# Kernel optimization log

Measured on AMD Instinct MI355X. Metric: run time of the kernel, lower is better.

The kernel has to match this reference:

```python
import jax, jax.numpy as jnp
import numpy as np

SEQ_LEN = 4096
D_IN = 2048
D_OUT = 2048
DROPOUT_P = 0.5


def setup_inputs() -> dict:
    key = jax.random.key(0)
    kx, kq, kk, kv = jax.random.split(key, 4)
    return {
        "x": jax.random.normal(kx, (SEQ_LEN, D_IN), dtype=jnp.float32),
        "W_query": jax.random.uniform(kq, (D_IN, D_OUT), dtype=jnp.float32),
        "W_key": jax.random.uniform(kk, (D_IN, D_OUT), dtype=jnp.float32),
        "W_value": jax.random.uniform(kv, (D_IN, D_OUT), dtype=jnp.float32),
    }


def reference(x, W_query, W_key, W_value):
    # projections: [S, d_in] @ [d_in, d_out] -> [S, d_out]
    queries = x @ W_query
    keys = x @ W_key
    values = x @ W_value
    # full score matrix [S, S]
    attn_scores = queries @ keys.T
    S = attn_scores.shape[0]
    causal_mask = jnp.triu(jnp.ones((S, S), dtype=bool), k=1)
    masked = jnp.where(causal_mask, -jnp.inf, attn_scores)
    scale = jnp.sqrt(jnp.asarray(keys.shape[-1], dtype=masked.dtype))
    attn_weights = jax.nn.softmax(masked / scale, axis=1)
    # dropout p=0.5 (train mode), inverted scaling, deterministic key
    keep = jax.random.bernoulli(jax.random.key(42), 1.0 - DROPOUT_P, attn_weights.shape)
    attn_weights = jnp.where(keep, attn_weights / (1.0 - DROPOUT_P), 0.0)
    context_vec = attn_weights @ values  # [S, d_out]
    return context_vec
```

## Files before the change

### kernel.cpp

```cpp
#include <hip/hip_runtime.h>
#include <cstdint>
#include <cstddef>
#include <cmath>

#define SEQ 4096
#define DM  2048
#define NSC ((SEQ / 128) * (SEQ / 128 + 1) / 2)

typedef unsigned int u32;
typedef unsigned short u16;
typedef __attribute__((ext_vector_type(8))) short bf16x8;
typedef __attribute__((ext_vector_type(4))) float f32x4;
typedef __attribute__((ext_vector_type(16))) float f32x16;

__device__ __forceinline__ u16 f2bf(float f) {
  u32 u = __float_as_uint(f);
  return (u16)((u + 0x7FFFu + ((u >> 16) & 1u)) >> 16);
}
__device__ __forceinline__ float bf2f(u16 h) { return __uint_as_float(((u32)h) << 16); }

__device__ __forceinline__ u32 rotl32(u32 x, int r) { return (x << r) | (x >> (32 - r)); }

__device__ __forceinline__ void tf2x32(u32 c0, u32 c1, u32& o0, u32& o1) {
  const u32 k0 = 0u, k1 = 42u, k2 = 0x1BD11BDAu ^ 0u ^ 42u;
  u32 x0 = c0 + k0;
  u32 x1 = c1 + k1;
#define TFR(r) { x0 += x1; x1 = rotl32(x1, (r)); x1 ^= x0; }
  TFR(13) TFR(15) TFR(26) TFR(6)   x0 += k1; x1 += k2 + 1u;
  TFR(17) TFR(29) TFR(16) TFR(24)  x0 += k2; x1 += k0 + 2u;
  TFR(13) TFR(15) TFR(26) TFR(6)   x0 += k0; x1 += k1 + 3u;
  TFR(17) TFR(29) TFR(16) TFR(24)  x0 += k1; x1 += k2 + 4u;
  TFR(13) TFR(15) TFR(26) TFR(6)   x0 += k2; x1 += k0 + 5u;
#undef TFR
  o0 = x0; o1 = x1;
}

__device__ __forceinline__ bool dropout_keep(u32 idx) {
  u32 a, b; tf2x32(0u, idx, a, b);
  return (((a ^ b) & 0x80000000u) == 0u);
}

__device__ __forceinline__ void g2l16(const void* g, void* l) {
  __builtin_amdgcn_global_load_lds((const __attribute__((address_space(1))) u32*)g,
                                   (__attribute__((address_space(3))) u32*)l, 16, 0, 0);
}

#define MFMA16(a, b, c) __builtin_amdgcn_mfma_f32_16x16x32_bf16(a, b, c, 0, 0, 0)
#define MFMA32(a, b, c) __builtin_amdgcn_mfma_f32_32x32x16_bf16(a, b, c, 0, 0, 0)


__device__ __forceinline__ void gemm_core_split(
    const u16* __restrict__ Ah, const u16* __restrict__ AlFT,
    const u16* __restrict__ Bh, const u16* __restrict__ BlFT,
    int lda, int ldb, int rowBlock, int colBlock, int kmax,
    f32x16 (&acc)[2][2], u16* smem)
{
  u16* Als = smem;
  u16* Bls = smem + 8192;
  const int tid  = threadIdx.x;
  const int wid  = tid >> 6;
  const int lane = tid & 63;
  const int wr   = (wid & 1) << 6;
  const int wc   = (wid >> 1) << 6;
  const int l31  = lane & 31;
  const int lh   = lane >> 5;
  const int srow = wid * 32 + (lane >> 2);
  const int skol = (((lane & 3) ^ ((lane >> 3) & 3)) << 3);
  const int KA16 = lda >> 4, KB16 = ldb >> 4;
  const int rtA0 = (rowBlock >> 5) + ((wid & 1) << 1);
  const int rtB0 = (colBlock >> 5) + ((wid >> 1) << 1);
  const int swz  = (l31 >> 1) & 3;

  const f32x16 zero = {0.f,0.f,0.f,0.f,0.f,0.f,0.f,0.f,0.f,0.f,0.f,0.f,0.f,0.f,0.f,0.f};
#pragma unroll
  for (int i = 0; i < 2; ++i)
#pragma unroll
    for (int j = 0; j < 2; ++j) acc[i][j] = zero;

  for (int kb = 0; kb < kmax; kb += 64) {
#pragma unroll
    for (int h = 0; h < 2; ++h)
#pragma unroll
      for (int t = 0; t < 2; ++t) {
        const size_t ga = (size_t)(rowBlock + srow + t * 16) * lda + kb + h * 32 + skol;
        const size_t gb = (size_t)(colBlock + srow + t * 16) * ldb + kb + h * 32 + skol;
        const int lo = h * 4096 + (wid * 32 + t * 16) * 32;
        g2l16(Ah + ga, &Als[lo]);
        g2l16(Bh + gb, &Bls[lo]);
      }
    __syncthreads();

#pragma unroll
    for (int q = 0; q < 4; ++q) {
      const int h = q >> 1, s = q & 1;
      const int kt16 = (kb >> 4) + q;
      const int cl = s * 2 + lh;
      bf16x8 ah[2], bh[2], al[2], bl[2];
#pragma unroll
      for (int r = 0; r < 2; ++r) {
        const int rowA = wr + r * 32 + l31;
        const int rowB = wc + r * 32 + l31;
        ah[r] = *(const bf16x8*)&Als[h * 4096 + rowA * 32 + ((cl ^ swz) << 3)];
        bh[r] = *(const bf16x8*)&Bls[h * 4096 + rowB * 32 + ((cl ^ swz) << 3)];
        al[r] = *(const bf16x8*)(AlFT + (((size_t)(rtA0 + r) * KA16 + kt16) * 64 + lane) * 8);
        bl[r] = *(const bf16x8*)(BlFT + (((size_t)(rtB0 + r) * KB16 + kt16) * 64 + lane) * 8);
      }
#pragma unroll
      for (int r = 0; r < 2; ++r)
#pragma unroll
        for (int c = 0; c < 2; ++c) {
          acc[r][c] = MFMA32(ah[r], bh[c], acc[r][c]);
          acc[r][c] = MFMA32(ah[r], bl[c], acc[r][c]);
          acc[r][c] = MFMA32(al[r], bh[c], acc[r][c]);
        }
    }
    __syncthreads();
  }
}

__device__ __forceinline__ void gemm_core(
    const u16* __restrict__ Ah, const u16* __restrict__ Bh,
    int lda, int ldb, int rowBlock, int colBlock, int kmax,
    f32x4 (&acc)[4][4], u16* smem)
{
  u16* Als = smem;
  u16* Bls = smem + 8192;
  const int tid  = threadIdx.x;
  const int wid  = tid >> 6;
  const int lane = tid & 63;
  const int wr   = (wid & 1) << 6;
  const int wc   = (wid >> 1) << 6;
  const int lrow = lane & 15;
  const int lk   = (((lane >> 4) ^ ((lrow >> 1) & 3)) << 3);
  const int srow = wid * 32 + (lane >> 2);
  const int skol = (((lane & 3) ^ ((lane >> 3) & 3)) << 3);

  const f32x4 zero = {0.f, 0.f, 0.f, 0.f};
#pragma unroll
  for (int i = 0; i < 4; ++i)
#pragma unroll
    for (int j = 0; j < 4; ++j) acc[i][j] = zero;

  for (int kb = 0; kb < kmax; kb += 64) {
#pragma unroll
    for (int h = 0; h < 2; ++h)
#pragma unroll
      for (int t = 0; t < 2; ++t) {
        const size_t ga = (size_t)(rowBlock + srow + t * 16) * lda + kb + h * 32 + skol;
        const size_t gb = (size_t)(colBlock + srow + t * 16) * ldb + kb + h * 32 + skol;
        const int lo = h * 4096 + (wid * 32 + t * 16) * 32;
        g2l16(Ah + ga, &Als[lo]);
        g2l16(Bh + gb, &Bls[lo]);
      }
    __syncthreads();

#pragma unroll
    for (int h = 0; h < 2; ++h) {
      bf16x8 ah[4], bh[4];
#pragma unroll
      for (int r = 0; r < 4; ++r) {
        ah[r] = *(const bf16x8*)&Als[h * 4096 + (wr + r * 16 + lrow) * 32 + lk];
        bh[r] = *(const bf16x8*)&Bls[h * 4096 + (wc + r * 16 + lrow) * 32 + lk];
      }
#pragma unroll
      for (int r = 0; r < 4; ++r)
#pragma unroll
        for (int c = 0; c < 4; ++c)
          acc[r][c] = MFMA16(ah[r], bh[c], acc[r][c]);
    }
    __syncthreads();
  }
}

__global__ __launch_bounds__(256) void k_split_all(
    const float* __restrict__ X, u16* __restrict__ Xh, u16* __restrict__ Xl,
    const float* __restrict__ Wq, const float* __restrict__ Wk, const float* __restrict__ Wv,
    u16* __restrict__ Wqh, u16* __restrict__ Wql,
    u16* __restrict__ Wkh, u16* __restrict__ Wkl, u16* __restrict__ Wvh) {
  __shared__ float t[64][65];
  const int bid = blockIdx.x;
  const int tid = threadIdx.x;
  const int wid = tid >> 6, lane = tid & 63;

  if (bid < 4096) {
    const int kt16 = bid & 127;
    const int rt32 = (bid >> 7) * 4 + wid;
    const int row = rt32 * 32 + (lane & 31);
    const int col = kt16 * 16 + ((lane >> 5) << 3);
    const float* src = X + (size_t)row * DM + col;
    const float4 v0 = *(const float4*)src;
    const float4 v1 = *(const float4*)(src + 4);
    float v[8] = {v0.x, v0.y, v0.z, v0.w, v1.x, v1.y, v1.z, v1.w};
    u16 h[8], l[8];
#pragma unroll
    for (int j = 0; j < 8; ++j) {
      h[j] = f2bf(v[j]);
      l[j] = f2bf(v[j] - bf2f(h[j]));
    }
    u16* hp = Xh + (size_t)row * DM + col;
    *(ushort4*)hp = *(ushort4*)&h[0];
    *(ushort4*)(hp + 4) = *(ushort4*)&h[4];
    u16* lp = Xl + (((size_t)rt32 * 128 + kt16) * 64 + lane) * 8;
    *(ushort4*)lp = *(ushort4*)&l[0];
    *(ushort4*)(lp + 4) = *(ushort4*)&l[4];
    return;
  }

  const int r = bid - 4096;
  const int z = r >> 10;
  const int rem = r & 1023;
  const int n0 = (rem & 31) * 64, k0 = (rem >> 5) * 64;
  const float* W = (z == 0) ? Wq : (z == 1) ? Wk : Wv;
  u16* Oh = (z == 0) ? Wqh : (z == 1) ? Wkh : Wvh;
  u16* Ol = (z == 0) ? Wql : Wkl;
  const int tx = tid & 63, ty = tid >> 6;
#pragma unroll
  for (int i = 0; i < 16; ++i)
    t[ty * 16 + i][tx] = W[(size_t)(k0 + ty * 16 + i) * DM + n0 + tx];
  __syncthreads();
  {
    const int nl = tid >> 2, kc = (tid & 3) * 16;
    u16 h[16];
#pragma unroll
    for (int i = 0; i < 16; ++i) h[i] = f2bf(t[kc + i][nl]);
    u16* hp = Oh + (size_t)(n0 + nl) * DM + k0 + kc;
#pragma unroll
    for (int i = 0; i < 4; ++i) *(ushort4*)(hp + i * 4) = *(ushort4*)&h[i * 4];
  }
  if (z < 2) {
#pragma unroll
    for (int tt = 0; tt < 2; ++tt) {
      const int idx = wid * 2 + tt;
      const int rt = idx >> 2, kt = idx & 3;
      const int nl = rt * 32 + (lane & 31);
      const int kc = kt * 16 + ((lane >> 5) << 3);
      u16 l[8];
#pragma unroll
      for (int j = 0; j < 8; ++j) {
        const float v = t[kc + j][nl];
        l[j] = f2bf(v - bf2f(f2bf(v)));
      }
      const int rtg = (n0 >> 5) + rt, ktg = (k0 >> 4) + kt;
      u16* lp = Ol + (((size_t)rtg * (DM / 16) + ktg) * 64 + lane) * 8;
      *(ushort4*)lp = *(ushort4*)&l[0];
      *(ushort4*)(lp + 4) = *(ushort4*)&l[4];
    }
  }
}

__global__ __launch_bounds__(512, 2) void k_proj_qk(
    const u16* __restrict__ Xh, const u16* __restrict__ Xl,
    const u16* __restrict__ Wqh, const u16* __restrict__ Wql,
    const u16* __restrict__ Wkh, const u16* __restrict__ Wkl,
    u16* __restrict__ Qh, u16* __restrict__ Ql,
    u16* __restrict__ Kh, u16* __restrict__ Kl, float rscaleQ)
{
  __shared__ __align__(16) u16 smem[65536];
  const int z = blockIdx.z;
  const u16* __restrict__ Bw = z ? Wkh : Wqh;
  const u16* __restrict__ Bl = z ? Wkl : Wql;
  u16* __restrict__ Oh = z ? Kh : Qh;
  u16* __restrict__ Ol = z ? Kl : Ql;
  const float rs = z ? 1.0f : rscaleQ;

  const int rowBlock = blockIdx.y * 256;
  const int colBlock = blockIdx.x * 256;
  const int tid  = threadIdx.x;
  const int wid  = tid >> 6, lane = tid & 63;
  const int wm   = wid >> 2, wn = wid & 3;
  const int l31  = lane & 31, lh = lane >> 5;
  const int srow = tid >> 2, schunk = tid & 3;
  const int sko  = ((schunk ^ ((srow >> 1) & 3)) << 3);
  const int rkey = (l31 >> 1) & 3;
  const int rtA0 = (rowBlock >> 5) + wm * 4;
  const int rtB0 = (colBlock >> 5) + wn * 2;

  f32x16 acc[4][2];
  {
    const f32x16 z16 = {0.f,0.f,0.f,0.f,0.f,0.f,0.f,0.f,0.f,0.f,0.f,0.f,0.f,0.f,0.f,0.f};
#pragma unroll
    for (int r = 0; r < 4; ++r)
#pragma unroll
      for (int c = 0; c < 2; ++c) acc[r][c] = z16;
  }
  bf16x8 alo0[4], blo0[2], alo1[4], blo1[2];

#define QK_STG(hh, pp) { \
    g2l16(Xh + (size_t)(rowBlock + (pp)*128 + srow) * DM + kbn + (hh)*32 + sko, \
          &smem[bufN + (hh)*8192 + (pp)*4096 + tid*8]); \
    g2l16(Bw + (size_t)(colBlock + (pp)*128 + srow) * DM + kbn + (hh)*32 + sko, \
          &smem[bufN + 16384 + (hh)*8192 + (pp)*4096 + tid*8]); }

#define QK_LO(AV, BV, kt) { \
    const int kk_ = (kt); \
    _Pragma("unroll") for (int r_ = 0; r_ < 4; ++r_) \
      AV[r_] = *(const bf16x8*)(Xl + (((size_t)(rtA0 + r_) * 128 + kk_) * 64 + lane) * 8); \
    _Pragma("unroll") for (int c_ = 0; c_ < 2; ++c_) \
      BV[c_] = *(const bf16x8*)(Bl + (((size_t)(rtB0 + c_) * 128 + kk_) * 64 + lane) * 8); }

#define QK_PH(qq, ALC, BLC, ALN, BLN, STMT, ktn) { \
    __builtin_amdgcn_sched_barrier(0); \
    QK_LO(ALN, BLN, ktn); \
    __builtin_amdgcn_sched_barrier(0); \
    STMT; \
    bf16x8 ah[4], bh[2]; \
    const int cl_ = ((qq) & 1) * 2 + lh; \
    const int hx_ = (qq) >> 1; \
    _Pragma("unroll") for (int r_ = 0; r_ < 4; ++r_) \
      ah[r_] = *(const bf16x8*)&smem[bufC + ((hx_*256 + wm*128 + r_*32 + l31) << 5) + ((cl_ ^ rkey) << 3)]; \
    _Pragma("unroll") for (int c_ = 0; c_ < 2; ++c_) \
      bh[c_] = *(const bf16x8*)&smem[bufC + 16384 + ((hx_*256 + wn*64 + c_*32 + l31) << 5) + ((cl_ ^ rkey) << 3)]; \
    __builtin_amdgcn_s_setprio(1); \
    _Pragma("unroll") for (int r_ = 0; r_ < 4; ++r_) \
      _Pragma("unroll") for (int c_ = 0; c_ < 2; ++c_) { \
        acc[r_][c_] = MFMA32(ah[r_], bh[c_], acc[r_][c_]); \
        acc[r_][c_] = MFMA32(ah[r_], BLC[c_], acc[r_][c_]); \
        acc[r_][c_] = MFMA32(ALC[r_], bh[c_], acc[r_][c_]); } \
    __builtin_amdgcn_s_setprio(0); }

  {
    const size_t kbn = 0; const int bufN = 0;
    QK_STG(0,0) QK_STG(0,1) QK_STG(1,0) QK_STG(1,1)
  }
  QK_LO(alo0, blo0, 0);
  asm volatile("s_waitcnt vmcnt(0)" ::: "memory");
  __builtin_amdgcn_s_barrier();

  for (int t = 0; t < 32; ++t) {
    const int bufC = (t & 1) << 15;
    const int bufN = bufC ^ 32768;
    const size_t kbn = (size_t)(t + 1) * 64;
    const bool more = (t < 31);
    const int g4 = t * 4;
    QK_PH(0, alo0, blo0, alo1, blo1, if (more) { QK_STG(0,0) QK_STG(0,1) }, g4 + 1)
    QK_PH(1, alo1, blo1, alo0, blo0, if (more) { QK_STG(1,0) QK_STG(1,1) }, g4 + 2)
    QK_PH(2, alo0, blo0, alo1, blo1, ;, g4 + 3)
    QK_PH(3, alo1, blo1, alo0, blo0, ;, (g4 + 4 < 128 ? g4 + 4 : 127))
    asm volatile("s_waitcnt vmcnt(0)" ::: "memory");
    __builtin_amdgcn_s_barrier();
  }
#undef QK_PH
#undef QK_LO
#undef QK_STG

  __syncthreads();
  u16* scr = smem + wid * 8192;
  const int r0g = rowBlock + wm * 128;
  const int c0g = colBlock + wn * 64;
#pragma unroll
  for (int r = 0; r < 4; ++r)
#pragma unroll
    for (int c = 0; c < 2; ++c) {
      const int colL = c * 32 + l31;
#pragma unroll
      for (int g = 0; g < 4; ++g)
#pragma unroll
        for (int e = 0; e < 4; ++e) {
          const int rowL = r * 32 + 8 * g + 4 * lh + e;
          const float v = acc[r][c][g * 4 + e] * rs;
          const u16 h = f2bf(v);
          Oh[(size_t)(r0g + rowL) * DM + c0g + colL] = h;
          scr[rowL * 64 + (((colL >> 3) ^ (rowL & 7)) << 3) + (colL & 7)] =
              f2bf(v - bf2f(h));
        }
    }
  asm volatile("s_waitcnt lgkmcnt(0)" ::: "memory");
  __builtin_amdgcn_sched_barrier(0);
#pragma unroll
  for (int rt = 0; rt < 4; ++rt)
#pragma unroll
    for (int kt = 0; kt < 4; ++kt) {
      const int rowL = rt * 32 + l31;
      const int cl2 = kt * 2 + lh;
      const bf16x8 v = *(const bf16x8*)&scr[rowL * 64 + ((cl2 ^ (rowL & 7)) << 3)];
      const int rtg = (rowBlock >> 5) + wm * 4 + rt;
      const int ktg = (colBlock >> 4) + wn * 4 + kt;
      *(bf16x8*)(Ol + (((size_t)rtg * 128 + ktg) * 64 + lane) * 8) = v;
    }
}

__global__ __launch_bounds__(512, 2) void k_proj_v(
    const u16* __restrict__ Xh, const u16* __restrict__ Wvh, u16* __restrict__ Vt)
{
  __shared__ __align__(16) u16 smem[49152];
  const int rowBlock = blockIdx.y * 256;
  const int colBlock = blockIdx.x * 128;
  const int tid  = threadIdx.x;
  const int wid  = tid >> 6, lane = tid & 63;
  const int wm   = wid >> 1, wn = wid & 1;
  const int l31  = lane & 31, lh = lane >> 5;
  const int srow = tid >> 2, schunk = tid & 3;
  const int sko  = ((schunk ^ ((srow >> 1) & 3)) << 3);
  const int rkey = (l31 >> 1) & 3;

  f32x16 acc[2][2];
  {
    const f32x16 z16 = {0.f,0.f,0.f,0.f,0.f,0.f,0.f,0.f,0.f,0.f,0.f,0.f,0.f,0.f,0.f,0.f};
#pragma unroll
    for (int r = 0; r < 2; ++r)
#pragma unroll
      for (int c = 0; c < 2; ++c) acc[r][c] = z16;
  }

#define V_STGA(hh, pp) g2l16(Xh + (size_t)(rowBlock + (pp)*128 + srow) * DM + kbn + (hh)*32 + sko, \
                             &smem[bufN + (hh)*8192 + (pp)*4096 + tid*8]);
#define V_STGB(hh)     g2l16(Wvh + (size_t)(colBlock + srow) * DM + kbn + (hh)*32 + sko, \
                             &smem[bufN + 16384 + (hh)*4096 + tid*8]);

#define V_PH(qq, STMT) { \
    __builtin_amdgcn_sched_barrier(0); \
    STMT; \
    bf16x8 ah[2], bh[2]; \
    const int cl_ = ((qq) & 1) * 2 + lh; \
    const int hx_ = (qq) >> 1; \
    _Pragma("unroll") for (int r_ = 0; r_ < 2; ++r_) \
      ah[r_] = *(const bf16x8*)&smem[bufC + ((hx_*256 + wm*64 + r_*32 + l31) << 5) + ((cl_ ^ rkey) << 3)]; \
    _Pragma("unroll") for (int c_ = 0; c_ < 2; ++c_) \
      bh[c_] = *(const bf16x8*)&smem[bufC + 16384 + ((hx_*128 + wn*64 + c_*32 + l31) << 5) + ((cl_ ^ rkey) << 3)]; \
    __builtin_amdgcn_s_setprio(1); \
    _Pragma("unroll") for (int r_ = 0; r_ < 2; ++r_) \
      _Pragma("unroll") for (int c_ = 0; c_ < 2; ++c_) \
        acc[r_][c_] = MFMA32(ah[r_], bh[c_], acc[r_][c_]); \
    __builtin_amdgcn_s_setprio(0); }

  {
    const size_t kbn = 0; const int bufN = 0;
    V_STGA(0,0) V_STGA(0,1) V_STGA(1,0) V_STGA(1,1) V_STGB(0) V_STGB(1)
  }
  asm volatile("s_waitcnt vmcnt(0)" ::: "memory");
  __builtin_amdgcn_s_barrier();

  for (int t = 0; t < 32; ++t) {
    const int bufC = (t & 1) * 24576;
    const int bufN = bufC ^ 24576;
    const size_t kbn = (size_t)(t + 1) * 64;
    const bool more = (t < 31);
    V_PH(0, if (more) { V_STGA(0,0) V_STGA(0,1) V_STGB(0) })
    V_PH(1, if (more) { V_STGA(1,0) V_STGA(1,1) V_STGB(1) })
    V_PH(2, ;)
    V_PH(3, ;)
    asm volatile("s_waitcnt vmcnt(0)" ::: "memory");
    __builtin_amdgcn_s_barrier();
  }
#undef V_PH
#undef V_STGB
#undef V_STGA

  const int vr0 = rowBlock + wm * 64;
#pragma unroll
  for (int r = 0; r < 2; ++r)
#pragma unroll
    for (int c = 0; c < 2; ++c) {
      const int col = colBlock + wn * 64 + c * 32 + l31;
#pragma unroll
      for (int g = 0; g < 4; ++g) {
        ushort4 pk;
        pk.x = f2bf(acc[r][c][g * 4 + 0]);
        pk.y = f2bf(acc[r][c][g * 4 + 1]);
        pk.z = f2bf(acc[r][c][g * 4 + 2]);
        pk.w = f2bf(acc[r][c][g * 4 + 3]);
        *(ushort4*)(Vt + (size_t)col * SEQ + vr0 + r * 32 + 8 * g + 4 * lh) = pk;
      }
    }
}

__global__ __launch_bounds__(256) void k_scores(
    const u16* __restrict__ Qh, const u16* __restrict__ Ql,
    const u16* __restrict__ Kh, const u16* __restrict__ Kl, float* __restrict__ S)
{
  __shared__ __align__(16) u16 smem[16384];
  const int bid = blockIdx.x;
  int by = (int)((sqrtf(8.0f * (float)bid + 1.0f) - 1.0f) * 0.5f);
  while ((by + 1) * (by + 2) / 2 <= bid) ++by;
  while (by * (by + 1) / 2 > bid) --by;
  const int bx = bid - by * (by + 1) / 2;

  f32x16 acc[2][2];
  gemm_core_split(Qh, Ql, Kh, Kl, DM, DM, by * 128, bx * 128, DM, acc, smem);

  const int lane = threadIdx.x & 63, wid = threadIdx.x >> 6;
  const int wr = (wid & 1) << 6, wc = (wid >> 1) << 6;
  const int l31 = lane & 31, lh = lane >> 5;
  const int r0 = by * 128 + wr, c0 = bx * 128 + wc;
#pragma unroll
  for (int r = 0; r < 2; ++r)
#pragma unroll
    for (int c = 0; c < 2; ++c) {
      const int col = c0 + c * 32 + l31;
#pragma unroll
      for (int g = 0; g < 4; ++g)
#pragma unroll
        for (int e = 0; e < 4; ++e) {
          const int row = r0 + r * 32 + 4 * lh + e + 8 * g;
          S[(size_t)row * SEQ + col] = acc[r][c][g * 4 + e];
        }
    }
}

__global__ __launch_bounds__(256) void k_softmax_dropout(const float* __restrict__ S,
                                                         u16* __restrict__ P) {
  const int row = blockIdx.x;
  const int n = row + 1;
  const int nt = (n + 1023) >> 10;
  const int tid = threadIdx.x;
  __shared__ float buf[SEQ];
  __shared__ float red[4];
  __shared__ float bcast;
  const float* srow = S + (size_t)row * SEQ;

  float lmax = -INFINITY;
  for (int t = 0; t < nt; ++t) {
    int j4 = tid + t * 256;
    float4 v = *(const float4*)(srow + (size_t)j4 * 4);
    int b = j4 * 4;
    float x0 = (b + 0 < n) ? v.x : -INFINITY;
    float x1 = (b + 1 < n) ? v.y : -INFINITY;
    float x2 = (b + 2 < n) ? v.z : -INFINITY;
    float x3 = (b + 3 < n) ? v.w : -INFINITY;
    buf[b + 0] = x0; buf[b + 1] = x1; buf[b + 2] = x2; buf[b + 3] = x3;
    lmax = fmaxf(lmax, fmaxf(fmaxf(x0, x1), fmaxf(x2, x3)));
  }
  for (int off = 32; off > 0; off >>= 1) lmax = fmaxf(lmax, __shfl_down(lmax, off, 64));
  if ((tid & 63) == 0) red[tid >> 6] = lmax;
  __syncthreads();
  if (tid == 0) bcast = fmaxf(fmaxf(red[0], red[1]), fmaxf(red[2], red[3]));
  __syncthreads();
  const float m = bcast;

  float lsum = 0.f;
  for (int t = 0; t < nt; ++t) {
    int b = (tid + t * 256) * 4;
    float e0 = expf(buf[b + 0] - m);
    float e1 = expf(buf[b + 1] - m);
    float e2 = expf(buf[b + 2] - m);
    float e3 = expf(buf[b + 3] - m);
    buf[b + 0] = e0; buf[b + 1] = e1; buf[b + 2] = e2; buf[b + 3] = e3;
    lsum += (e0 + e1) + (e2 + e3);
  }
  for (int off = 32; off > 0; off >>= 1) lsum += __shfl_down(lsum, off, 64);
  if ((tid & 63) == 0) red[tid >> 6] = lsum;
  __syncthreads();
  if (tid == 0) bcast = (red[0] + red[1]) + (red[2] + red[3]);
  __syncthreads();
  const float total = bcast;

  u16* prow = P + (size_t)row * SEQ;
  const int zeroEnd = ((row >> 7) + 1) << 7;
  for (int j = tid; j < zeroEnd; j += 256) {
    float out = 0.f;
    if (j < n) {
      const float w = buf[j] / total;
      out = dropout_keep((u32)(row * SEQ + j)) ? w * 2.0f : 0.f;
    }
    prow[j] = f2bf(out);
  }
}

__global__ __launch_bounds__(256) void k_pv(const u16* __restrict__ P,
                                            const u16* __restrict__ Vt,
                                            float* __restrict__ O) {
  __shared__ __align__(16) u16 smem[16384];
  const int by = (SEQ / 128 - 1) - blockIdx.y;
  f32x4 acc[4][4];
  gemm_core(P, Vt, SEQ, SEQ, by * 128, blockIdx.x * 128, (by + 1) * 128, acc, smem);

  const int lane = threadIdx.x & 63, wid = threadIdx.x >> 6;
  const int r0 = by * 128 + ((wid & 1) << 6) + ((lane >> 4) << 2);
  const int c0 = blockIdx.x * 128 + ((wid >> 1) << 6) + (lane & 15);
#pragma unroll
  for (int r = 0; r < 4; ++r)
#pragma unroll
    for (int c = 0; c < 4; ++c)
#pragma unroll
      for (int e = 0; e < 4; ++e)
        O[(size_t)(r0 + r * 16 + e) * DM + (c0 + c * 16)] = acc[r][c][e];
}

extern "C" void kernel_launch(void* const* d_in, const int* in_sizes, int n_in,
                              void* d_out, int out_size, void* d_ws, size_t ws_size,
                              hipStream_t stream) {
  const float* x  = (const float*)d_in[0];
  const float* Wq = (const float*)d_in[1];
  const float* Wk = (const float*)d_in[2];
  const float* Wv = (const float*)d_in[3];

  const size_t PL = (size_t)SEQ * DM;
  const size_t WL = (size_t)DM * DM;
  u16* base = (u16*)d_ws;
  u16* Qh = base;
  u16* Ql = Qh + PL;
  u16* Kh = Ql + PL;
  u16* Kl = Kh + PL;
  u16* Vt = Kl + PL;
  u16* P  = base;
  u16* regA = Vt + PL;
  u16* Xh  = regA;
  u16* Xl  = Xh + PL;
  u16* Wqh = Xl + PL;
  u16* Wql = Wqh + WL;
  u16* Wkh = Wql + WL;
  u16* Wkl = Wkh + WL;
  u16* Wvh = Wkl + WL;
  float* S = (float*)regA;

  const float rscale = 1.0f / sqrtf(2048.0f);
  k_split_all<<<dim3(4096 + 3 * 1024), dim3(256), 0, stream>>>(
      x, Xh, Xl, Wq, Wk, Wv, Wqh, Wql, Wkh, Wkl, Wvh);
  k_proj_qk<<<dim3(DM / 256, SEQ / 256, 2), dim3(512), 0, stream>>>(
      Xh, Xl, Wqh, Wql, Wkh, Wkl, Qh, Ql, Kh, Kl, rscale);
  k_proj_v<<<dim3(DM / 128, SEQ / 256), dim3(512), 0, stream>>>(Xh, Wvh, Vt);
  k_scores<<<dim3(NSC), dim3(256), 0, stream>>>(Qh, Ql, Kh, Kl, S);
  k_softmax_dropout<<<dim3(SEQ), dim3(256), 0, stream>>>(S, P);
  k_pv<<<dim3(DM / 128, SEQ / 128), dim3(256), 0, stream>>>(P, Vt, (float*)d_out);
}
```

Baseline: 614.7 us.

## Stage low-half operands through LDS and retile scores kernel to 256x128 pipelined blocks

The QK projection kernel stops loading the bf16 low-half fragments of X and W directly from global memory into registers and instead stages them into LDS with global_load_lds, next to the high halves. It uses a double-buffered 32-wide k-step with the copies spread across two phases. The scores kernel is rewritten from the generic split GEMM core into a dedicated 512-thread, 256x128-tile kernel with the same double-buffered LDS pipeline. It also uses a new triangular block mapping that launches 272 blocks. The aim is to replace uncoalesced per-wave global loads with asynchronous LDS staging and to overlap copies with MFMA work. The cost is more LDS per block and more barriers per k-iteration.

```diff
diff --git a/kernel.cpp b/kernel.cpp
--- a/kernel.cpp
+++ b/kernel.cpp
@@ -5,7 +5,6 @@
 
 #define SEQ 4096
 #define DM  2048
-#define NSC ((SEQ / 128) * (SEQ / 128 + 1) / 2)
 
 typedef unsigned int u32;
 typedef unsigned short u16;
@@ -48,75 +47,6 @@
 #define MFMA16(a, b, c) __builtin_amdgcn_mfma_f32_16x16x32_bf16(a, b, c, 0, 0, 0)
 #define MFMA32(a, b, c) __builtin_amdgcn_mfma_f32_32x32x16_bf16(a, b, c, 0, 0, 0)
 
-
-__device__ __forceinline__ void gemm_core_split(
-    const u16* __restrict__ Ah, const u16* __restrict__ AlFT,
-    const u16* __restrict__ Bh, const u16* __restrict__ BlFT,
-    int lda, int ldb, int rowBlock, int colBlock, int kmax,
-    f32x16 (&acc)[2][2], u16* smem)
-{
-  u16* Als = smem;
-  u16* Bls = smem + 8192;
-  const int tid  = threadIdx.x;
-  const int wid  = tid >> 6;
-  const int lane = tid & 63;
-  const int wr   = (wid & 1) << 6;
-  const int wc   = (wid >> 1) << 6;
-  const int l31  = lane & 31;
-  const int lh   = lane >> 5;
-  const int srow = wid * 32 + (lane >> 2);
-  const int skol = (((lane & 3) ^ ((lane >> 3) & 3)) << 3);
-  const int KA16 = lda >> 4, KB16 = ldb >> 4;
-  const int rtA0 = (rowBlock >> 5) + ((wid & 1) << 1);
-  const int rtB0 = (colBlock >> 5) + ((wid >> 1) << 1);
-  const int swz  = (l31 >> 1) & 3;
-
-  const f32x16 zero = {0.f,0.f,0.f,0.f,0.f,0.f,0.f,0.f,0.f,0.f,0.f,0.f,0.f,0.f,0.f,0.f};
-#pragma unroll
-  for (int i = 0; i < 2; ++i)
-#pragma unroll
-    for (int j = 0; j < 2; ++j) acc[i][j] = zero;
-
-  for (int kb = 0; kb < kmax; kb += 64) {
-#pragma unroll
-    for (int h = 0; h < 2; ++h)
-#pragma unroll
-      for (int t = 0; t < 2; ++t) {
-        const size_t ga = (size_t)(rowBlock + srow + t * 16) * lda + kb + h * 32 + skol;
-        const size_t gb = (size_t)(colBlock + srow + t * 16) * ldb + kb + h * 32 + skol;
-        const int lo = h * 4096 + (wid * 32 + t * 16) * 32;
-        g2l16(Ah + ga, &Als[lo]);
-        g2l16(Bh + gb, &Bls[lo]);
-      }
-    __syncthreads();
-
-#pragma unroll
-    for (int q = 0; q < 4; ++q) {
-      const int h = q >> 1, s = q & 1;
-      const int kt16 = (kb >> 4) + q;
-      const int cl = s * 2 + lh;
-      bf16x8 ah[2], bh[2], al[2], bl[2];
-#pragma unroll
-      for (int r = 0; r < 2; ++r) {
-        const int rowA = wr + r * 32 + l31;
-        const int rowB = wc + r * 32 + l31;
-        ah[r] = *(const bf16x8*)&Als[h * 4096 + rowA * 32 + ((cl ^ swz) << 3)];
-        bh[r] = *(const bf16x8*)&Bls[h * 4096 + rowB * 32 + ((cl ^ swz) << 3)];
-        al[r] = *(const bf16x8*)(AlFT + (((size_t)(rtA0 + r) * KA16 + kt16) * 64 + lane) * 8);
-        bl[r] = *(const bf16x8*)(BlFT + (((size_t)(rtB0 + r) * KB16 + kt16) * 64 + lane) * 8);
-      }
-#pragma unroll
-      for (int r = 0; r < 2; ++r)
-#pragma unroll
-        for (int c = 0; c < 2; ++c) {
-          acc[r][c] = MFMA32(ah[r], bh[c], acc[r][c]);
-          acc[r][c] = MFMA32(ah[r], bl[c], acc[r][c]);
-          acc[r][c] = MFMA32(al[r], bh[c], acc[r][c]);
-        }
-    }
-    __syncthreads();
-  }
-}
 
 __device__ __forceinline__ void gemm_core(
     const u16* __restrict__ Ah, const u16* __restrict__ Bh,
@@ -272,8 +202,6 @@
   const int srow = tid >> 2, schunk = tid & 3;
   const int sko  = ((schunk ^ ((srow >> 1) & 3)) << 3);
   const int rkey = (l31 >> 1) & 3;
-  const int rtA0 = (rowBlock >> 5) + wm * 4;
-  const int rtB0 = (colBlock >> 5) + wn * 2;
 
   f32x16 acc[4][2];
   {
@@ -283,65 +211,63 @@
 #pragma unroll
       for (int c = 0; c < 2; ++c) acc[r][c] = z16;
   }
-  bf16x8 alo0[4], blo0[2], alo1[4], blo1[2];
-
-#define QK_STG(hh, pp) { \
-    g2l16(Xh + (size_t)(rowBlock + (pp)*128 + srow) * DM + kbn + (hh)*32 + sko, \
-          &smem[bufN + (hh)*8192 + (pp)*4096 + tid*8]); \
-    g2l16(Bw + (size_t)(colBlock + (pp)*128 + srow) * DM + kbn + (hh)*32 + sko, \
-          &smem[bufN + 16384 + (hh)*8192 + (pp)*4096 + tid*8]); }
-
-#define QK_LO(AV, BV, kt) { \
-    const int kk_ = (kt); \
+
+#define P_STG_AHI(pp) g2l16(Xh + (size_t)(rowBlock + (pp)*128 + srow) * DM + kbn + sko, \
+                            &smem[bufN + (pp)*4096 + tid*8]);
+#define P_STG_BHI(pp) g2l16(Bw + (size_t)(colBlock + (pp)*128 + srow) * DM + kbn + sko, \
+                            &smem[bufN + 8192 + (pp)*4096 + tid*8]);
+#define P_STG_ALO(ss) { const int idx_ = (ss)*8 + wid; \
+    g2l16(Xl + ((size_t)((rowBlock >> 5) + (idx_ >> 1)) * 128 + (kbn >> 4) + (idx_ & 1)) * 512 + lane*8, \
+          &smem[bufN + 16384 + idx_*512 + lane*8]); }
+#define P_STG_BLO(ss) { const int idx_ = (ss)*8 + wid; \
+    g2l16(Bl + ((size_t)((colBlock >> 5) + (idx_ >> 1)) * 128 + (kbn >> 4) + (idx_ & 1)) * 512 + lane*8, \
+          &smem[bufN + 24576 + idx_*512 + lane*8]); }
+
+#define P_PHASE(qq) { \
+    bf16x8 ah[4], bh[2], al[4], bl[2]; \
+    const int cl_ = (qq)*2 + lh; \
     _Pragma("unroll") for (int r_ = 0; r_ < 4; ++r_) \
-      AV[r_] = *(const bf16x8*)(Xl + (((size_t)(rtA0 + r_) * 128 + kk_) * 64 + lane) * 8); \
+      ah[r_] = *(const bf16x8*)&smem[bufC + ((wm*128 + r_*32 + l31) << 5) + ((cl_ ^ rkey) << 3)]; \
     _Pragma("unroll") for (int c_ = 0; c_ < 2; ++c_) \
-      BV[c_] = *(const bf16x8*)(Bl + (((size_t)(rtB0 + c_) * 128 + kk_) * 64 + lane) * 8); }
-
-#define QK_PH(qq, ALC, BLC, ALN, BLN, STMT, ktn) { \
-    __builtin_amdgcn_sched_barrier(0); \
-    QK_LO(ALN, BLN, ktn); \
-    __builtin_amdgcn_sched_barrier(0); \
-    STMT; \
-    bf16x8 ah[4], bh[2]; \
-    const int cl_ = ((qq) & 1) * 2 + lh; \
-    const int hx_ = (qq) >> 1; \
+      bh[c_] = *(const bf16x8*)&smem[bufC + 8192 + ((wn*64 + c_*32 + l31) << 5) + ((cl_ ^ rkey) << 3)]; \
     _Pragma("unroll") for (int r_ = 0; r_ < 4; ++r_) \
-      ah[r_] = *(const bf16x8*)&smem[bufC + ((hx_*256 + wm*128 + r_*32 + l31) << 5) + ((cl_ ^ rkey) << 3)]; \
+      al[r_] = *(const bf16x8*)&smem[bufC + 16384 + ((wm*4 + r_)*2 + (qq))*512 + lane*8]; \
     _Pragma("unroll") for (int c_ = 0; c_ < 2; ++c_) \
-      bh[c_] = *(const bf16x8*)&smem[bufC + 16384 + ((hx_*256 + wn*64 + c_*32 + l31) << 5) + ((cl_ ^ rkey) << 3)]; \
+      bl[c_] = *(const bf16x8*)&smem[bufC + 24576 + ((wn*2 + c_)*2 + (qq))*512 + lane*8]; \
     __builtin_amdgcn_s_setprio(1); \
     _Pragma("unroll") for (int r_ = 0; r_ < 4; ++r_) \
       _Pragma("unroll") for (int c_ = 0; c_ < 2; ++c_) { \
         acc[r_][c_] = MFMA32(ah[r_], bh[c_], acc[r_][c_]); \
-        acc[r_][c_] = MFMA32(ah[r_], BLC[c_], acc[r_][c_]); \
-        acc[r_][c_] = MFMA32(ALC[r_], bh[c_], acc[r_][c_]); } \
+        acc[r_][c_] = MFMA32(ah[r_], bl[c_], acc[r_][c_]); \
+        acc[r_][c_] = MFMA32(al[r_], bh[c_], acc[r_][c_]); } \
     __builtin_amdgcn_s_setprio(0); }
 
   {
     const size_t kbn = 0; const int bufN = 0;
-    QK_STG(0,0) QK_STG(0,1) QK_STG(1,0) QK_STG(1,1)
-  }
-  QK_LO(alo0, blo0, 0);
+    P_STG_AHI(0) P_STG_AHI(1) P_STG_BHI(0) P_STG_BHI(1)
+    P_STG_ALO(0) P_STG_ALO(1) P_STG_BLO(0) P_STG_BLO(1)
+  }
   asm volatile("s_waitcnt vmcnt(0)" ::: "memory");
   __builtin_amdgcn_s_barrier();
 
-  for (int t = 0; t < 32; ++t) {
+  for (int t = 0; t < 64; ++t) {
     const int bufC = (t & 1) << 15;
     const int bufN = bufC ^ 32768;
-    const size_t kbn = (size_t)(t + 1) * 64;
-    const bool more = (t < 31);
-    const int g4 = t * 4;
-    QK_PH(0, alo0, blo0, alo1, blo1, if (more) { QK_STG(0,0) QK_STG(0,1) }, g4 + 1)
-    QK_PH(1, alo1, blo1, alo0, blo0, if (more) { QK_STG(1,0) QK_STG(1,1) }, g4 + 2)
-    QK_PH(2, alo0, blo0, alo1, blo1, ;, g4 + 3)
-    QK_PH(3, alo1, blo1, alo0, blo0, ;, (g4 + 4 < 128 ? g4 + 4 : 127))
+    const size_t kbn = (size_t)(t + 1) * 32;
+    if (t < 63) { P_STG_AHI(0) P_STG_AHI(1) P_STG_BHI(0) P_STG_BHI(1) }
+    __builtin_amdgcn_sched_barrier(0);
+    P_PHASE(0)
+    if (t < 63) { P_STG_ALO(0) P_STG_ALO(1) P_STG_BLO(0) P_STG_BLO(1) }
+    __builtin_amdgcn_sched_barrier(0);
+    P_PHASE(1)
     asm volatile("s_waitcnt vmcnt(0)" ::: "memory");
     __builtin_amdgcn_s_barrier();
   }
-#undef QK_PH
-#undef QK_LO
-#undef QK_STG
+#undef P_PHASE
+#undef P_STG_BLO
+#undef P_STG_ALO
+#undef P_STG_BHI
+#undef P_STG_AHI
 
   __syncthreads();
   u16* scr = smem + wid * 8192;
@@ -464,24 +390,93 @@
     }
 }
 
-__global__ __launch_bounds__(256) void k_scores(
+__global__ __launch_bounds__(512, 2) void k_scores(
     const u16* __restrict__ Qh, const u16* __restrict__ Ql,
     const u16* __restrict__ Kh, const u16* __restrict__ Kl, float* __restrict__ S)
 {
-  __shared__ __align__(16) u16 smem[16384];
+  __shared__ __align__(16) u16 smem[49152];
   const int bid = blockIdx.x;
-  int by = (int)((sqrtf(8.0f * (float)bid + 1.0f) - 1.0f) * 0.5f);
-  while ((by + 1) * (by + 2) / 2 <= bid) ++by;
-  while (by * (by + 1) / 2 > bid) --by;
-  const int bx = bid - by * (by + 1) / 2;
+  int by = (int)((sqrtf(4.0f * (float)bid + 1.0f) - 1.0f) * 0.5f);
+  while ((by + 1) * (by + 2) <= bid) ++by;
+  while (by * (by + 1) > bid) --by;
+  const int bx = bid - by * (by + 1);
+  const int rowBlock = by * 256, colBlock = bx * 128;
+
+  const int tid  = threadIdx.x;
+  const int wid  = tid >> 6, lane = tid & 63;
+  const int wm   = wid >> 1, wn = wid & 1;
+  const int l31  = lane & 31, lh = lane >> 5;
+  const int srow = tid >> 2, schunk = tid & 3;
+  const int sko  = ((schunk ^ ((srow >> 1) & 3)) << 3);
+  const int rkey = (l31 >> 1) & 3;
 
   f32x16 acc[2][2];
-  gemm_core_split(Qh, Ql, Kh, Kl, DM, DM, by * 128, bx * 128, DM, acc, smem);
-
-  const int lane = threadIdx.x & 63, wid = threadIdx.x >> 6;
-  const int wr = (wid & 1) << 6, wc = (wid >> 1) << 6;
-  const int l31 = lane & 31, lh = lane >> 5;
-  const int r0 = by * 128 + wr, c0 = bx * 128 + wc;
+  {
+    const f32x16 z16 = {0.f,0.f,0.f,0.f,0.f,0.f,0.f,0.f,0.f,0.f,0.f,0.f,0.f,0.f,0.f,0.f};
+#pragma unroll
+    for (int r = 0; r < 2; ++r)
+#pragma unroll
+      for (int c = 0; c < 2; ++c) acc[r][c] = z16;
+  }
+
+#define S_STG_AHI(pp) g2l16(Qh + (size_t)(rowBlock + (pp)*128 + srow) * DM + kbn + sko, \
+                            &smem[bufN + (pp)*4096 + tid*8]);
+#define S_STG_BHI     g2l16(Kh + (size_t)(colBlock + srow) * DM + kbn + sko, \
+                            &smem[bufN + 8192 + tid*8]);
+#define S_STG_ALO(ss) { const int idx_ = (ss)*8 + wid; \
+    g2l16(Ql + ((size_t)((rowBlock >> 5) + (idx_ >> 1)) * 128 + (kbn >> 4) + (idx_ & 1)) * 512 + lane*8, \
+          &smem[bufN + 12288 + idx_*512 + lane*8]); }
+#define S_STG_BLO     { const int idx_ = wid; \
+    g2l16(Kl + ((size_t)((colBlock >> 5) + (idx_ >> 1)) * 128 + (kbn >> 4) + (idx_ & 1)) * 512 + lane*8, \
+          &smem[bufN + 20480 + idx_*512 + lane*8]); }
+
+#define S_PHASE(qq) { \
+    bf16x8 ah[2], bh[2], al[2], bl[2]; \
+    const int cl_ = (qq)*2 + lh; \
+    _Pragma("unroll") for (int r_ = 0; r_ < 2; ++r_) \
+      ah[r_] = *(const bf16x8*)&smem[bufC + ((wm*64 + r_*32 + l31) << 5) + ((cl_ ^ rkey) << 3)]; \
+    _Pragma("unroll") for (int c_ = 0; c_ < 2; ++c_) \
+      bh[c_] = *(const bf16x8*)&smem[bufC + 8192 + ((wn*64 + c_*32 + l31) << 5) + ((cl_ ^ rkey) << 3)]; \
+    _Pragma("unroll") for (int r_ = 0; r_ < 2; ++r_) \
+      al[r_] = *(const bf16x8*)&smem[bufC + 12288 + ((wm*2 + r_)*2 + (qq))*512 + lane*8]; \
+    _Pragma("unroll") for (int c_ = 0; c_ < 2; ++c_) \
+      bl[c_] = *(const bf16x8*)&smem[bufC + 20480 + ((wn*2 + c_)*2 + (qq))*512 + lane*8]; \
+    __builtin_amdgcn_s_setprio(1); \
+    _Pragma("unroll") for (int r_ = 0; r_ < 2; ++r_) \
+      _Pragma("unroll") for (int c_ = 0; c_ < 2; ++c_) { \
+        acc[r_][c_] = MFMA32(ah[r_], bh[c_], acc[r_][c_]); \
+        acc[r_][c_] = MFMA32(ah[r_], bl[c_], acc[r_][c_]); \
+        acc[r_][c_] = MFMA32(al[r_], bh[c_], acc[r_][c_]); } \
+    __builtin_amdgcn_s_setprio(0); }
+
+  {
+    const size_t kbn = 0; const int bufN = 0;
+    S_STG_AHI(0) S_STG_AHI(1) S_STG_BHI
+    S_STG_ALO(0) S_STG_ALO(1) S_STG_BLO
+  }
+  asm volatile("s_waitcnt vmcnt(0)" ::: "memory");
+  __builtin_amdgcn_s_barrier();
+
+  for (int t = 0; t < 64; ++t) {
+    const int bufC = (t & 1) * 24576;
+    const int bufN = bufC ^ 24576;
+    const size_t kbn = (size_t)(t + 1) * 32;
+    if (t < 63) { S_STG_AHI(0) S_STG_AHI(1) S_STG_BHI }
+    __builtin_amdgcn_sched_barrier(0);
+    S_PHASE(0)
+    if (t < 63) { S_STG_ALO(0) S_STG_ALO(1) S_STG_BLO }
+    __builtin_amdgcn_sched_barrier(0);
+    S_PHASE(1)
+    asm volatile("s_waitcnt vmcnt(0)" ::: "memory");
+    __builtin_amdgcn_s_barrier();
+  }
+#undef S_PHASE
+#undef S_STG_BLO
+#undef S_STG_ALO
+#undef S_STG_BHI
+#undef S_STG_AHI
+
+  const int r0 = rowBlock + wm * 64, c0 = colBlock + wn * 64;
 #pragma unroll
   for (int r = 0; r < 2; ++r)
 #pragma unroll
@@ -491,7 +486,7 @@
       for (int g = 0; g < 4; ++g)
 #pragma unroll
         for (int e = 0; e < 4; ++e) {
-          const int row = r0 + r * 32 + 4 * lh + e + 8 * g;
+          const int row = r0 + r * 32 + 8 * g + 4 * lh + e;
           S[(size_t)row * SEQ + col] = acc[r][c][g * 4 + e];
         }
     }
@@ -609,7 +604,7 @@
   k_proj_qk<<<dim3(DM / 256, SEQ / 256, 2), dim3(512), 0, stream>>>(
       Xh, Xl, Wqh, Wql, Wkh, Wkl, Qh, Ql, Kh, Kl, rscale);
   k_proj_v<<<dim3(DM / 128, SEQ / 256), dim3(512), 0, stream>>>(Xh, Wvh, Vt);
-  k_scores<<<dim3(NSC), dim3(256), 0, stream>>>(Qh, Ql, Kh, Kl, S);
+  k_scores<<<dim3(272), dim3(512), 0, stream>>>(Qh, Ql, Kh, Kl, S);
   k_softmax_dropout<<<dim3(SEQ), dim3(256), 0, stream>>>(S, P);
   k_pv<<<dim3(DM / 128, SEQ / 128), dim3(256), 0, stream>>>(P, Vt, (float*)d_out);
 }
```

Result: no change. 610.4 us (-0.7%).
